# Optimization experiments

Hardware: AMD Instinct MI355X
Metric: run time of the kernel (lower is better)

The kernel has to match this reference:

```python
import jax, jax.numpy as jnp
import numpy as np

B, T_FEAT, D = 16, 4096, 512
T_TOK = 1024


def setup_inputs() -> dict:
    key = jax.random.key(0)
    k1, k2, k3, k4, k5 = jax.random.split(key, 5)
    encoded_feats = jax.random.normal(k1, (B, T_FEAT, D), dtype=jnp.float32)
    encoded_feat_lengths = jax.random.randint(k2, (B,), 1, T_FEAT + 1).astype(jnp.int32)
    asr_token_ids = jax.random.randint(k3, (B, T_TOK), 0, 32000).astype(jnp.int64)
    asr_token_lengths = jax.random.randint(k4, (B,), 1, T_TOK + 1).astype(jnp.int32)
    # fractional [start, end] alignments in [0,1], sorted so start <= end
    asr_token_alignments = jnp.sort(jax.random.uniform(k5, (B, T_TOK, 2), dtype=jnp.float32), axis=-1)
    return {
        "encoded_feats": encoded_feats,
        "encoded_feat_lengths": encoded_feat_lengths,
        "asr_token_ids": asr_token_ids,
        "asr_token_lengths": asr_token_lengths,
        "asr_token_alignments": asr_token_alignments,
    }


def reference(encoded_feats, encoded_feat_lengths, asr_token_ids, asr_token_lengths, asr_token_alignments):
    # alignments: fractional positions scaled to frame indices, truncated like torch .int()
    align = (asr_token_alignments * encoded_feat_lengths[:, None, None].astype(jnp.float32)).astype(jnp.int32)  # [B, Tt, 2]
    idx = jnp.arange(encoded_feats.shape[1], dtype=jnp.int32)  # [Tf]
    # token validity mask (~make_pad_mask)
    token_mask = jnp.arange(asr_token_ids.shape[1], dtype=jnp.int32)[None, :] < asr_token_lengths[:, None]  # [B, Tt]
    # [B, Tt, Tf] segment membership mask (inclusive [start, end])
    mask = token_mask[:, :, None] & (idx[None, None, :] >= align[:, :, 0:1]) & (idx[None, None, :] <= align[:, :, 1:2])
    maskf = mask.astype(encoded_feats.dtype)
    # masked sum without materializing [B, Tt, Tf, D]
    sums = jnp.einsum("btf,bfd->btd", maskf, encoded_feats)  # [B, Tt, D]
    counts = jnp.sum(maskf, axis=-1, keepdims=True)  # [B, Tt, 1]
    segmented_feats = jnp.nan_to_num(sums / counts)
    return segmented_feats, asr_token_lengths
```

## Files before the change

### kernel.cpp

```cpp
#include <hip/hip_runtime.h>

namespace {

constexpr int kB  = 16;
constexpr int kF  = 4096;
constexpr int kD  = 512;
constexpr int kTT = 1024;
constexpr int kC  = 64;
constexpr int kJ  = 8;
constexpr int kD4 = kD / 4;

__device__ inline void acc4(float4& a, const float4& v) {
    a.x += v.x; a.y += v.y; a.z += v.z; a.w += v.w;
}
__device__ inline void sub4(float4& a, const float4& v) {
    a.x -= v.x; a.y -= v.y; a.z -= v.z; a.w -= v.w;
}

__global__ void chunk_ps8_k(const float4* __restrict__ feats,
                            const int* __restrict__ flens,
                            float4* __restrict__ PS8) {
    int tid = blockIdx.x * blockDim.x + threadIdx.x;
    int q = tid & (kD4 - 1);
    int c = (tid >> 7) & (kC - 1);
    int b = tid >> 13;
    int flen = flens[b];
    int base_row = c * 64;
    float4* o = PS8 + ((size_t)((b * kC + c) * kJ)) * kD4 + q;
    if (base_row >= flen) {
        float4 z = make_float4(0.f, 0.f, 0.f, 0.f);
#pragma unroll
        for (int j = 0; j < kJ; ++j) o[(size_t)j * kD4] = z;
        return;
    }
    const float4* p = feats + ((size_t)(b * kF + base_row)) * kD4 + q;
    float4 r = make_float4(0.f, 0.f, 0.f, 0.f);
    if (base_row + 64 <= flen) {
        for (int j = 0; j < kJ; ++j) {
#pragma unroll
            for (int i = 0; i < 8; ++i) acc4(r, p[(size_t)(j * 8 + i) * kD4]);
            o[(size_t)j * kD4] = r;
        }
    } else {
        int nvalid = flen - base_row;
        for (int j = 0; j < kJ; ++j) {
            for (int i = 0; i < 8; ++i) {
                int row = j * 8 + i;
                if (row < nvalid) acc4(r, p[(size_t)row * kD4]);
            }
            o[(size_t)j * kD4] = r;
        }
    }
}

__global__ void chunk_offsets_k(const float* __restrict__ PS8,
                                float* __restrict__ O64) {
    int tid = blockIdx.x * blockDim.x + threadIdx.x;
    int d = tid & (kD - 1);
    int b = tid >> 9;
    float r = 0.f;
    for (int c = 0; c < kC; ++c) {
        O64[((size_t)(b * kC + c)) * kD + d] = r;
        r += PS8[((size_t)((b * kC + c) * kJ + (kJ - 1))) * kD + d];
    }
}

__device__ inline float4 prefix_at(const float4* __restrict__ feats,
                                   const float4* __restrict__ PS8,
                                   const float4* __restrict__ O64,
                                   int b, int r, int q, int flen) {
    int c = r >> 6;
    int j = (r >> 3) & 7;
    int t = r & 7;
    int blk_start = c * 64 + j * 8;
    float4 acc = O64[((size_t)(b * kC + c)) * kD4 + q];
    const float4* base = feats + ((size_t)(b * kF + blk_start)) * kD4 + q;
    if (t >= 4) {
        acc4(acc, PS8[((size_t)((b * kC + c) * kJ + j)) * kD4 + q]);
        int lim = flen - blk_start;
        if (lim > 8) lim = 8;
        for (int i = t + 1; i < lim; ++i) sub4(acc, base[(size_t)i * kD4]);
    } else {
        if (j > 0) acc4(acc, PS8[((size_t)((b * kC + c) * kJ + j - 1)) * kD4 + q]);
        for (int i = 0; i <= t; ++i) acc4(acc, base[(size_t)i * kD4]);
    }
    return acc;
}

__global__ void gather_k(const float4* __restrict__ feats,
                         const float4* __restrict__ PS8,
                         const float4* __restrict__ O64,
                         const int* __restrict__ flens,
                         const int* __restrict__ tlens,
                         const float2* __restrict__ aligns,
                         float4* __restrict__ out,
                         float* __restrict__ out_lens) {
    int blk = blockIdx.x;
    int t = blk & (kTT - 1);
    int b = blk >> 10;
    int q = threadIdx.x;
    int tlen = tlens[b];
    int flen = flens[b];
    float fl = (float)flen;
    float2 a = aligns[blk];
    int s = (int)(a.x * fl);
    int e = (int)(a.y * fl);
    if (e > kF - 1) e = kF - 1;
    int cnt = e - s + 1;
    float4 res = make_float4(0.f, 0.f, 0.f, 0.f);
    if (t < tlen && cnt > 0 && s < kF) {
        float4 hi = prefix_at(feats, PS8, O64, b, e, q, flen);
        float4 lo = make_float4(0.f, 0.f, 0.f, 0.f);
        if (s > 0) lo = prefix_at(feats, PS8, O64, b, s - 1, q, flen);
        float fc = (float)cnt;
        res = make_float4((hi.x - lo.x) / fc, (hi.y - lo.y) / fc,
                          (hi.z - lo.z) / fc, (hi.w - lo.w) / fc);
    }
    out[((size_t)blk) * kD4 + q] = res;
    if (t == 0 && q == 0) out_lens[b] = (float)tlen;
}

__global__ void direct_k(const float4* __restrict__ feats,
                         const int* __restrict__ flens,
                         const int* __restrict__ tlens,
                         const float2* __restrict__ aligns,
                         float4* __restrict__ out,
                         float* __restrict__ out_lens) {
    int blk = blockIdx.x;
    int t = blk & (kTT - 1);
    int b = blk >> 10;
    int q = threadIdx.x;
    int tlen = tlens[b];
    float fl = (float)flens[b];
    float2 a = aligns[blk];
    int s = (int)(a.x * fl);
    int e = (int)(a.y * fl);
    if (e > kF - 1) e = kF - 1;
    int cnt = e - s + 1;
    float4 res = make_float4(0.f, 0.f, 0.f, 0.f);
    if (t < tlen && cnt > 0 && s < kF) {
        const float4* p = feats + ((size_t)(b * kF + s)) * kD4 + q;
        float4 r = make_float4(0.f, 0.f, 0.f, 0.f);
        for (int i = 0; i < cnt; ++i) acc4(r, p[(size_t)i * kD4]);
        float fc = (float)cnt;
        res = make_float4(r.x / fc, r.y / fc, r.z / fc, r.w / fc);
    }
    out[((size_t)blk) * kD4 + q] = res;
    if (t == 0 && q == 0) out_lens[b] = (float)tlen;
}

}

extern "C" void kernel_launch(void* const* d_in, const int* in_sizes, int n_in,
                              void* d_out, int out_size, void* d_ws, size_t ws_size,
                              hipStream_t stream) {
    const float4* feats  = (const float4*)d_in[0];
    const int*    flens  = (const int*)d_in[1];
    const int*    tlens  = (const int*)d_in[3];
    const float2* aligns = (const float2*)d_in[4];

    float* out      = (float*)d_out;
    float* out_lens = out + (size_t)kB * kTT * kD;

    const size_t needPS8 = (size_t)kB * kC * kJ * kD * sizeof(float);
    const size_t needO64 = (size_t)kB * kC * kD * sizeof(float);

    if (ws_size >= needPS8 + needO64) {
        float4* PS8 = (float4*)d_ws;
        float4* O64 = (float4*)((char*)d_ws + needPS8);

        int n1 = kB * kC * kD4;
        chunk_ps8_k<<<n1 / 256, 256, 0, stream>>>(feats, flens, PS8);
        int n2 = kB * kD;
        chunk_offsets_k<<<n2 / 256, 256, 0, stream>>>((const float*)PS8, (float*)O64);
        gather_k<<<kB * kTT, kD4, 0, stream>>>(feats, PS8, O64, flens, tlens, aligns,
                                               (float4*)out, out_lens);
    } else {
        direct_k<<<kB * kTT, kD4, 0, stream>>>(feats, flens, tlens, aligns,
                                               (float4*)out, out_lens);
    }
}
```

Before: 48.06 us.

## Store per-row chunk-local prefix sums in fp16 for single-lookup gather

The scan kernel now writes a per-row prefix sum within each 64-row chunk, packed as fp16, instead of fp32 partial sums every 8 rows. Gather then needs just one fp16 row plus the chunk offset per endpoint, rather than partial sums plus up to four raw feature rows. This trades a larger write in the first pass, and reduced-precision prefix values, for much less gather traffic. It also needs a larger workspace, and the code falls back to the direct path if that workspace is unavailable.

```diff
diff --git a/kernel.cpp b/kernel.cpp
--- a/kernel.cpp
+++ b/kernel.cpp
@@ -1,4 +1,5 @@
 #include <hip/hip_runtime.h>
+#include <hip/hip_fp16.h>
 
 namespace {
 
@@ -7,53 +8,62 @@
 constexpr int kD  = 512;
 constexpr int kTT = 1024;
 constexpr int kC  = 64;
-constexpr int kJ  = 8;
 constexpr int kD4 = kD / 4;
 
 __device__ inline void acc4(float4& a, const float4& v) {
     a.x += v.x; a.y += v.y; a.z += v.z; a.w += v.w;
 }
-__device__ inline void sub4(float4& a, const float4& v) {
-    a.x -= v.x; a.y -= v.y; a.z -= v.z; a.w -= v.w;
+
+__device__ inline ushort4 pack_h4(const float4& v) {
+    ushort4 u;
+    u.x = __half_as_ushort(__float2half_rn(v.x));
+    u.y = __half_as_ushort(__float2half_rn(v.y));
+    u.z = __half_as_ushort(__float2half_rn(v.z));
+    u.w = __half_as_ushort(__float2half_rn(v.w));
+    return u;
 }
 
-__global__ void chunk_ps8_k(const float4* __restrict__ feats,
-                            const int* __restrict__ flens,
-                            float4* __restrict__ PS8) {
+__device__ inline float4 unpack_h4(const ushort4& u) {
+    return make_float4(__half2float(__ushort_as_half(u.x)),
+                       __half2float(__ushort_as_half(u.y)),
+                       __half2float(__ushort_as_half(u.z)),
+                       __half2float(__ushort_as_half(u.w)));
+}
+
+__global__ void chunk_prefix_k(const float4* __restrict__ feats,
+                               const int* __restrict__ flens,
+                               ushort4* __restrict__ Pc,
+                               float4* __restrict__ S) {
     int tid = blockIdx.x * blockDim.x + threadIdx.x;
     int q = tid & (kD4 - 1);
     int c = (tid >> 7) & (kC - 1);
     int b = tid >> 13;
     int flen = flens[b];
     int base_row = c * 64;
-    float4* o = PS8 + ((size_t)((b * kC + c) * kJ)) * kD4 + q;
-    if (base_row >= flen) {
-        float4 z = make_float4(0.f, 0.f, 0.f, 0.f);
-#pragma unroll
-        for (int j = 0; j < kJ; ++j) o[(size_t)j * kD4] = z;
-        return;
-    }
-    const float4* p = feats + ((size_t)(b * kF + base_row)) * kD4 + q;
     float4 r = make_float4(0.f, 0.f, 0.f, 0.f);
-    if (base_row + 64 <= flen) {
-        for (int j = 0; j < kJ; ++j) {
-#pragma unroll
-            for (int i = 0; i < 8; ++i) acc4(r, p[(size_t)(j * 8 + i) * kD4]);
-            o[(size_t)j * kD4] = r;
-        }
-    } else {
-        int nvalid = flen - base_row;
-        for (int j = 0; j < kJ; ++j) {
-            for (int i = 0; i < 8; ++i) {
-                int row = j * 8 + i;
-                if (row < nvalid) acc4(r, p[(size_t)row * kD4]);
+    int nval = flen - base_row;
+    size_t fbase = ((size_t)(b * kF + base_row)) * kD4 + q;
+    if (nval > 0) {
+        if (nval > 64) nval = 64;
+        const float4* p = feats + fbase;
+        ushort4* o = Pc + fbase;
+        if (nval == 64) {
+#pragma unroll 8
+            for (int i = 0; i < 64; ++i) {
+                acc4(r, p[(size_t)i * kD4]);
+                o[(size_t)i * kD4] = pack_h4(r);
             }
-            o[(size_t)j * kD4] = r;
+        } else {
+            for (int i = 0; i < nval; ++i) {
+                acc4(r, p[(size_t)i * kD4]);
+                o[(size_t)i * kD4] = pack_h4(r);
+            }
         }
     }
+    S[((size_t)(b * kC + c)) * kD4 + q] = r;
 }
 
-__global__ void chunk_offsets_k(const float* __restrict__ PS8,
+__global__ void chunk_offsets_k(const float* __restrict__ S,
                                 float* __restrict__ O64) {
     int tid = blockIdx.x * blockDim.x + threadIdx.x;
     int d = tid & (kD - 1);
@@ -61,34 +71,20 @@
     float r = 0.f;
     for (int c = 0; c < kC; ++c) {
         O64[((size_t)(b * kC + c)) * kD + d] = r;
-        r += PS8[((size_t)((b * kC + c) * kJ + (kJ - 1))) * kD + d];
+        r += S[((size_t)(b * kC + c)) * kD + d];
     }
 }
 
-__device__ inline float4 prefix_at(const float4* __restrict__ feats,
-                                   const float4* __restrict__ PS8,
+__device__ inline float4 prefix_at(const ushort4* __restrict__ Pc,
                                    const float4* __restrict__ O64,
-                                   int b, int r, int q, int flen) {
-    int c = r >> 6;
-    int j = (r >> 3) & 7;
-    int t = r & 7;
-    int blk_start = c * 64 + j * 8;
-    float4 acc = O64[((size_t)(b * kC + c)) * kD4 + q];
-    const float4* base = feats + ((size_t)(b * kF + blk_start)) * kD4 + q;
-    if (t >= 4) {
-        acc4(acc, PS8[((size_t)((b * kC + c) * kJ + j)) * kD4 + q]);
-        int lim = flen - blk_start;
-        if (lim > 8) lim = 8;
-        for (int i = t + 1; i < lim; ++i) sub4(acc, base[(size_t)i * kD4]);
-    } else {
-        if (j > 0) acc4(acc, PS8[((size_t)((b * kC + c) * kJ + j - 1)) * kD4 + q]);
-        for (int i = 0; i <= t; ++i) acc4(acc, base[(size_t)i * kD4]);
-    }
+                                   int b, int r, int q) {
+    float4 acc = O64[((size_t)(b * kC + (r >> 6))) * kD4 + q];
+    float4 p = unpack_h4(Pc[((size_t)(b * kF + r)) * kD4 + q]);
+    acc4(acc, p);
     return acc;
 }
 
-__global__ void gather_k(const float4* __restrict__ feats,
-                         const float4* __restrict__ PS8,
+__global__ void gather_k(const ushort4* __restrict__ Pc,
                          const float4* __restrict__ O64,
                          const int* __restrict__ flens,
                          const int* __restrict__ tlens,
@@ -109,9 +105,13 @@
     int cnt = e - s + 1;
     float4 res = make_float4(0.f, 0.f, 0.f, 0.f);
     if (t < tlen && cnt > 0 && s < kF) {
-        float4 hi = prefix_at(feats, PS8, O64, b, e, q, flen);
+        int er = e;      if (er > flen - 1) er = flen - 1;
+        float4 hi = prefix_at(Pc, O64, b, er, q);
         float4 lo = make_float4(0.f, 0.f, 0.f, 0.f);
-        if (s > 0) lo = prefix_at(feats, PS8, O64, b, s - 1, q, flen);
+        if (s > 0) {
+            int sr = s - 1; if (sr > flen - 1) sr = flen - 1;
+            lo = prefix_at(Pc, O64, b, sr, q);
+        }
         float fc = (float)cnt;
         res = make_float4((hi.x - lo.x) / fc, (hi.y - lo.y) / fc,
                           (hi.z - lo.z) / fc, (hi.w - lo.w) / fc);
@@ -162,18 +162,20 @@
     float* out      = (float*)d_out;
     float* out_lens = out + (size_t)kB * kTT * kD;
 
-    const size_t needPS8 = (size_t)kB * kC * kJ * kD * sizeof(float);
-    const size_t needO64 = (size_t)kB * kC * kD * sizeof(float);
+    const size_t needPc  = (size_t)kB * kF * kD * sizeof(unsigned short);
+    const size_t needS   = (size_t)kB * kC * kD * sizeof(float);
+    const size_t needO64 = needS;
 
-    if (ws_size >= needPS8 + needO64) {
-        float4* PS8 = (float4*)d_ws;
-        float4* O64 = (float4*)((char*)d_ws + needPS8);
+    if (ws_size >= needPc + needS + needO64) {
+        ushort4* Pc  = (ushort4*)d_ws;
+        float4*  S   = (float4*)((char*)d_ws + needPc);
+        float4*  O64 = (float4*)((char*)d_ws + needPc + needS);
 
         int n1 = kB * kC * kD4;
-        chunk_ps8_k<<<n1 / 256, 256, 0, stream>>>(feats, flens, PS8);
+        chunk_prefix_k<<<n1 / 256, 256, 0, stream>>>(feats, flens, Pc, S);
         int n2 = kB * kD;
-        chunk_offsets_k<<<n2 / 256, 256, 0, stream>>>((const float*)PS8, (float*)O64);
-        gather_k<<<kB * kTT, kD4, 0, stream>>>(feats, PS8, O64, flens, tlens, aligns,
+        chunk_offsets_k<<<n2 / 256, 256, 0, stream>>>((const float*)S, (float*)O64);
+        gather_k<<<kB * kTT, kD4, 0, stream>>>(Pc, O64, flens, tlens, aligns,
                                                (float4*)out, out_lens);
     } else {
         direct_k<<<kB * kTT, kD4, 0, stream>>>(feats, flens, tlens, aligns,
```

Result: faster. 41.34 us (-14.0%).
